# Optimization experiments

Measured on AMD Instinct MI355X. Metric: run time of the kernel, lower is better.

Reference implementation:

```python
import jax, jax.numpy as jnp
import numpy as np

B, C_IN, H, W = 32, 128, 64, 64
C_OUT, KH, KW = 256, 3, 3


def setup_inputs() -> dict:
    key = jax.random.key(0)
    k1, k2, k3 = jax.random.split(key, 3)
    inputs = jax.random.normal(k1, (B, C_IN, H, W), dtype=jnp.float32)
    weights = jax.random.normal(k2, (C_OUT, C_IN, KH, KW), dtype=jnp.float32) * 0.05
    bias = jax.random.normal(k3, (C_OUT, 1), dtype=jnp.float32)
    return {"inputs": inputs, "weights": weights, "bias": bias}


def reference(inputs, weights, bias):
    # Direct 2D valid convolution, stride 1, padding 0 (module default).
    # output[b,o,i,j] = sum_{c,u,v} inputs[b,c,i+u,j+v] * weights[o,c,u,v] + bias[o]
    out = jax.lax.conv_general_dilated(
        inputs, weights,
        window_strides=(1, 1),
        padding="VALID",
        dimension_numbers=("NCHW", "OIHW", "NCHW"),
    )
    # bias has shape (C_out, 1); broadcast per output channel
    return out + bias.reshape(1, -1, 1, 1)
```

## Files before the change

### kernel.cpp

```cpp
#include <hip/hip_runtime.h>
#include <hip/hip_bf16.h>
#include <stdint.h>

#define BB   32
#define CIN  128
#define HH   64
#define WW   64
#define COUT 256
#define OHH  62
#define OWW  62
#define PIX_PER_B (OHH*OWW)
#define NPIX (BB*PIX_PER_B)
#define KTOT (9*CIN)
#define NKT  36
#define SLOT 24576

typedef __bf16 bf16x8 __attribute__((ext_vector_type(8)));
typedef float  f32x4  __attribute__((ext_vector_type(4)));
typedef uint16_t u16x8 __attribute__((ext_vector_type(8)));

__device__ __forceinline__ uint16_t f2bf(float f) {
    uint32_t u = __float_as_uint(f);
    uint32_t r = (u + 0x7FFFu + ((u >> 16) & 1u)) >> 16;
    return (uint16_t)r;
}

__device__ __forceinline__ void gload_lds16(const void* g, void* l) {
    __builtin_amdgcn_global_load_lds(
        (const __attribute__((address_space(1))) uint32_t*)g,
        (__attribute__((address_space(3))) uint32_t*)l, 16, 0, 0);
}

__global__ void __launch_bounds__(256) to_nhwc(const float* __restrict__ in,
                                               uint16_t* __restrict__ out) {
    int slab = blockIdx.x;
    int b = slab >> 6, h = slab & 63;
    int w  = threadIdx.x & 63;
    int cp = threadIdx.x >> 6;
    const float* src = in + (((size_t)b * CIN) * HH + h) * WW + w;
    uint16_t* dst = out + ((size_t)slab * WW + w) * CIN;
    #pragma unroll
    for (int it = 0; it < 4; ++it) {
        int c0 = cp * 32 + it * 8;
        u16x8 v;
        #pragma unroll
        for (int j = 0; j < 8; ++j) v[j] = f2bf(src[(c0 + j) * (HH * WW)]);
        *reinterpret_cast<u16x8*>(dst + c0) = v;
    }
}

__global__ void __launch_bounds__(256) pack_w(const float* __restrict__ w,
                                              uint16_t* __restrict__ out) {
    int idx = blockIdx.x * 256 + threadIdx.x;
    int o = idx / KTOT;
    int k = idx - o * KTOT;
    int uv = k >> 7, c = k & 127;
    out[idx] = f2bf(w[(o * CIN + c) * 9 + uv]);
}

__global__ void __launch_bounds__(256, 2) conv_k32(
        const uint16_t* __restrict__ Xg,
        const uint16_t* __restrict__ Wg,
        const float*    __restrict__ bias,
        float*          __restrict__ out)
{
    __shared__ char lds[3 * SLOT + 1024];
    int* pbase = (int*)(lds + 3 * SLOT);
    int* obase = pbase + 128;

    const int tid  = threadIdx.x;
    const int lane = tid & 63;
    const int wid  = tid >> 6;

    int bid = blockIdx.x;
    int xcd = bid & 7, lid = bid >> 3;
    int nt  = (xcd == 0 ? lid : 121 + (xcd - 1) * 120 + lid);

    if (tid < 128) {
        int n   = nt * 128 + tid;
        int b   = n / PIX_PER_B;
        int rem = n - b * PIX_PER_B;
        int oh  = rem / OWW;
        int ow  = rem - oh * OWW;
        pbase[tid] = ((b * 64 + oh) * 64 + ow) * 128;
        obase[tid] = b * (COUT * PIX_PER_B) + rem;
    }
    __syncthreads();

    const int cs   = (((tid & 3) ^ ((tid >> 3) & 3)) << 4);
    const int ldst = tid * 16;
    const char* aptr0 = (const char*)Wg + ((tid >> 2) + 0)   * (KTOT * 2) + cs;
    const char* aptr1 = (const char*)Wg + ((tid >> 2) + 64)  * (KTOT * 2) + cs;
    const char* aptr2 = (const char*)Wg + ((tid >> 2) + 128) * (KTOT * 2) + cs;
    const char* aptr3 = (const char*)Wg + ((tid >> 2) + 192) * (KTOT * 2) + cs;
    const char* xptr0 = (const char*)Xg + pbase[(tid >> 2)] * 2 + cs;
    const char* xptr1 = (const char*)Xg + pbase[(tid >> 2) + 64] * 2 + cs;

    const int wm = wid >> 1, wn = wid & 1;
    int aro[8], xro[4];
    #pragma unroll
    for (int mi = 0; mi < 8; ++mi) {
        int row = wm * 128 + mi * 16 + (lane & 15);
        aro[mi] = row * 64 + ((((lane >> 4) ^ ((row >> 1) & 3))) << 4);
    }
    #pragma unroll
    for (int nj = 0; nj < 4; ++nj) {
        int row = wn * 64 + nj * 16 + (lane & 15);
        xro[nj] = 16384 + row * 64 + ((((lane >> 4) ^ ((row >> 1) & 3))) << 4);
    }

    f32x4 acc[8][4] = {};

    auto stage = [&](int t, char* dst) {
        int uvv = t >> 2;
        int u   = (uvv * 11) >> 5;
        int v   = uvv - u * 3;
        int xo  = (u << 14) | (v << 8) | ((t & 3) << 6);
        gload_lds16(aptr0 + t * 64, dst + ldst);
        gload_lds16(aptr1 + t * 64, dst + 4096 + ldst);
        gload_lds16(aptr2 + t * 64, dst + 8192 + ldst);
        gload_lds16(aptr3 + t * 64, dst + 12288 + ldst);
        gload_lds16(xptr0 + xo, dst + 16384 + ldst);
        gload_lds16(xptr1 + xo, dst + 20480 + ldst);
    };

#define PHASE(T, S, S2, STG, VMC, BAR) do {                                    \
    char* _slot = lds + (S) * SLOT;                                            \
    if (STG) stage((T) + 2, lds + (S2) * SLOT);                                \
    bf16x8 af[8], xf[4];                                                       \
    _Pragma("unroll") for (int nj = 0; nj < 4; ++nj)                           \
        xf[nj] = *reinterpret_cast<const bf16x8*>(_slot + xro[nj]);            \
    _Pragma("unroll") for (int mi = 0; mi < 8; ++mi)                           \
        af[mi] = *reinterpret_cast<const bf16x8*>(_slot + aro[mi]);            \
    __builtin_amdgcn_s_setprio(1);                                             \
    _Pragma("unroll") for (int mi = 0; mi < 8; ++mi)                           \
      _Pragma("unroll") for (int nj = 0; nj < 4; ++nj)                         \
        acc[mi][nj] = __builtin_amdgcn_mfma_f32_16x16x32_bf16(                 \
            af[mi], xf[nj], acc[mi][nj], 0, 0, 0);                             \
    __builtin_amdgcn_s_setprio(0);                                             \
    if ((VMC) == 1) asm volatile("s_waitcnt vmcnt(6)" ::: "memory");           \
    else if ((VMC) == 2) asm volatile("s_waitcnt vmcnt(0)" ::: "memory");      \
    if (BAR) __builtin_amdgcn_s_barrier();                                     \
} while (0)

    stage(0, lds);
    stage(1, lds + SLOT);
    asm volatile("s_waitcnt vmcnt(6)" ::: "memory");
    __builtin_amdgcn_s_barrier();

    for (int i = 0; i < 11; ++i) {
        PHASE(3 * i + 0, 0, 2, 1, 1, 1);
        PHASE(3 * i + 1, 1, 0, 1, 1, 1);
        PHASE(3 * i + 2, 2, 1, 1, 1, 1);
    }
    PHASE(33, 0, 2, 1, 1, 1);
    PHASE(34, 1, 0, 0, 2, 1);
    PHASE(35, 2, 1, 0, 0, 0);
#undef PHASE

    #pragma unroll
    for (int mi = 0; mi < 8; ++mi) {
        int o = wm * 128 + mi * 16 + ((lane >> 4) << 2);
        #pragma unroll
        for (int reg = 0; reg < 4; ++reg) {
            float bv = bias[o + reg];
            #pragma unroll
            for (int nj = 0; nj < 4; ++nj) {
                int pl = wn * 64 + nj * 16 + (lane & 15);
                out[obase[pl] + (o + reg) * PIX_PER_B] = acc[mi][nj][reg] + bv;
            }
        }
    }
}

__global__ void __launch_bounds__(256) conv_naive(const float* __restrict__ in,
                                                  const float* __restrict__ w,
                                                  const float* __restrict__ bias,
                                                  float* __restrict__ out) {
    long idx = (long)blockIdx.x * 256 + threadIdx.x;
    int t = (int)idx;
    int ow = t % OWW; t /= OWW;
    int oh = t % OHH; t /= OHH;
    int o  = t % COUT;
    int b  = t / COUT;
    float s = bias[o];
    for (int c = 0; c < CIN; ++c)
        for (int u = 0; u < 3; ++u)
            for (int v = 0; v < 3; ++v)
                s += in[((b * CIN + c) * HH + oh + u) * WW + ow + v] *
                     w[((o * CIN + c) * 3 + u) * 3 + v];
    out[idx] = s;
}

extern "C" void kernel_launch(void* const* d_in, const int* in_sizes, int n_in,
                              void* d_out, int out_size, void* d_ws, size_t ws_size,
                              hipStream_t stream) {
    const float* in   = (const float*)d_in[0];
    const float* wt   = (const float*)d_in[1];
    const float* bias = (const float*)d_in[2];
    float* out = (float*)d_out;

    const size_t xg_elems = (size_t)BB * HH * WW * CIN;
    const size_t wg_elems = (size_t)COUT * KTOT;
    const size_t need = (xg_elems + wg_elems) * sizeof(uint16_t);

    if (ws_size < need) {
        long total = (long)BB * COUT * OHH * OWW;
        conv_naive<<<(int)((total + 255) / 256), 256, 0, stream>>>(in, wt, bias, out);
        return;
    }

    uint16_t* Xg = (uint16_t*)d_ws;
    uint16_t* Wg = Xg + xg_elems;

    to_nhwc<<<BB * HH, 256, 0, stream>>>(in, Xg);
    pack_w<<<(COUT * KTOT) / 256, 256, 0, stream>>>(wt, Wg);
    conv_k32<<<NPIX / 128, 256, 0, stream>>>(Xg, Wg, bias, out);
}
```

Baseline: 105.9 us.

## Load weight fragments directly from global into registers, stage only activations in LDS

Weight A-fragments are no longer staged through LDS. Each wave now loads its 8 bf16x8 weight fragments straight from global memory into double-buffered registers, one k-step ahead. LDS slots shrink to hold only the activation tile, and the vmcnt waits are retuned for the new mix of loads. This removes LDS traffic and capacity for weights, at the cost of more VGPRs, plus uncoalesced, redundant global or L2 weight reads, since the two waves sharing wm both fetch the same rows.

After: 183.7 us. 73.5% more time.

```diff
diff --git a/kernel.cpp b/kernel.cpp
--- a/kernel.cpp
+++ b/kernel.cpp
@@ -13,7 +13,7 @@
 #define NPIX (BB*PIX_PER_B)
 #define KTOT (9*CIN)
 #define NKT  36
-#define SLOT 24576
+#define SLOT 8192
 
 typedef __bf16 bf16x8 __attribute__((ext_vector_type(8)));
 typedef float  f32x4  __attribute__((ext_vector_type(4)));
@@ -58,7 +58,7 @@
     out[idx] = f2bf(w[(o * CIN + c) * 9 + uv]);
 }
 
-__global__ void __launch_bounds__(256, 2) conv_k32(
+__global__ void __launch_bounds__(256, 2) conv_areg(
         const uint16_t* __restrict__ Xg,
         const uint16_t* __restrict__ Wg,
         const float*    __restrict__ bias,
@@ -89,74 +89,78 @@
 
     const int cs   = (((tid & 3) ^ ((tid >> 3) & 3)) << 4);
     const int ldst = tid * 16;
-    const char* aptr0 = (const char*)Wg + ((tid >> 2) + 0)   * (KTOT * 2) + cs;
-    const char* aptr1 = (const char*)Wg + ((tid >> 2) + 64)  * (KTOT * 2) + cs;
-    const char* aptr2 = (const char*)Wg + ((tid >> 2) + 128) * (KTOT * 2) + cs;
-    const char* aptr3 = (const char*)Wg + ((tid >> 2) + 192) * (KTOT * 2) + cs;
-    const char* xptr0 = (const char*)Xg + pbase[(tid >> 2)] * 2 + cs;
-    const char* xptr1 = (const char*)Xg + pbase[(tid >> 2) + 64] * 2 + cs;
-
-    const int wm = wid >> 1, wn = wid & 1;
-    int aro[8], xro[4];
-    #pragma unroll
-    for (int mi = 0; mi < 8; ++mi) {
-        int row = wm * 128 + mi * 16 + (lane & 15);
-        aro[mi] = row * 64 + ((((lane >> 4) ^ ((row >> 1) & 3))) << 4);
-    }
-    #pragma unroll
-    for (int nj = 0; nj < 4; ++nj) {
-        int row = wn * 64 + nj * 16 + (lane & 15);
-        xro[nj] = 16384 + row * 64 + ((((lane >> 4) ^ ((row >> 1) & 3))) << 4);
-    }
-
-    f32x4 acc[8][4] = {};
-
-    auto stage = [&](int t, char* dst) {
+    const char* XgB = (const char*)Xg;
+    const char* xptr0 = XgB + pbase[(tid >> 2)] * 2 + cs;
+    const char* xptr1 = XgB + pbase[(tid >> 2) + 64] * 2 + cs;
+
+    auto stageX = [&](int t, char* dst) {
         int uvv = t >> 2;
         int u   = (uvv * 11) >> 5;
         int v   = uvv - u * 3;
         int xo  = (u << 14) | (v << 8) | ((t & 3) << 6);
-        gload_lds16(aptr0 + t * 64, dst + ldst);
-        gload_lds16(aptr1 + t * 64, dst + 4096 + ldst);
-        gload_lds16(aptr2 + t * 64, dst + 8192 + ldst);
-        gload_lds16(aptr3 + t * 64, dst + 12288 + ldst);
-        gload_lds16(xptr0 + xo, dst + 16384 + ldst);
-        gload_lds16(xptr1 + xo, dst + 20480 + ldst);
+        gload_lds16(xptr0 + xo, dst + ldst);
+        gload_lds16(xptr1 + xo, dst + 4096 + ldst);
     };
 
-#define PHASE(T, S, S2, STG, VMC, BAR) do {                                    \
-    char* _slot = lds + (S) * SLOT;                                            \
-    if (STG) stage((T) + 2, lds + (S2) * SLOT);                                \
-    bf16x8 af[8], xf[4];                                                       \
+    const int wm = wid >> 1, wn = wid & 1;
+    const char* ap = (const char*)Wg +
+                     (wm * 128 + (lane & 15)) * (KTOT * 2) + ((lane >> 4) << 4);
+
+    int xro[4];
+    #pragma unroll
+    for (int nj = 0; nj < 4; ++nj) {
+        int row = wn * 64 + nj * 16 + (lane & 15);
+        xro[nj] = row * 64 + ((((lane >> 4) ^ ((row >> 1) & 3))) << 4);
+    }
+
+    f32x4 acc[8][4] = {};
+    bf16x8 afA[8], afB[8];
+
+#define LOADA(T, AF) do {                                                      \
+    const char* _a = ap + (T) * 64;                                            \
+    _Pragma("unroll") for (int mi = 0; mi < 8; ++mi)                           \
+        AF[mi] = *reinterpret_cast<const bf16x8*>(_a + mi * 36864);            \
+} while (0)
+
+#define PH(T, S, S2, AFC, AFN, STG, ALD, VMC, BAR) do {                        \
+    if (STG) stageX((T) + 2, lds + (S2) * SLOT);                               \
+    if (ALD) LOADA((T) + 1, AFN);                                              \
+    bf16x8 xf[4];                                                              \
     _Pragma("unroll") for (int nj = 0; nj < 4; ++nj)                           \
-        xf[nj] = *reinterpret_cast<const bf16x8*>(_slot + xro[nj]);            \
-    _Pragma("unroll") for (int mi = 0; mi < 8; ++mi)                           \
-        af[mi] = *reinterpret_cast<const bf16x8*>(_slot + aro[mi]);            \
+        xf[nj] = *reinterpret_cast<const bf16x8*>(lds + (S) * SLOT + xro[nj]); \
+    asm volatile("s_waitcnt vmcnt(" #VMC ")" ::: "memory");                    \
     __builtin_amdgcn_s_setprio(1);                                             \
     _Pragma("unroll") for (int mi = 0; mi < 8; ++mi)                           \
       _Pragma("unroll") for (int nj = 0; nj < 4; ++nj)                         \
         acc[mi][nj] = __builtin_amdgcn_mfma_f32_16x16x32_bf16(                 \
-            af[mi], xf[nj], acc[mi][nj], 0, 0, 0);                             \
+            AFC[mi], xf[nj], acc[mi][nj], 0, 0, 0);                            \
     __builtin_amdgcn_s_setprio(0);                                             \
-    if ((VMC) == 1) asm volatile("s_waitcnt vmcnt(6)" ::: "memory");           \
-    else if ((VMC) == 2) asm volatile("s_waitcnt vmcnt(0)" ::: "memory");      \
     if (BAR) __builtin_amdgcn_s_barrier();                                     \
 } while (0)
 
-    stage(0, lds);
-    stage(1, lds + SLOT);
-    asm volatile("s_waitcnt vmcnt(6)" ::: "memory");
+    stageX(0, lds);
+    LOADA(0, afA);
+    stageX(1, lds + SLOT);
+    asm volatile("s_waitcnt vmcnt(2)" ::: "memory");
     __builtin_amdgcn_s_barrier();
 
-    for (int i = 0; i < 11; ++i) {
-        PHASE(3 * i + 0, 0, 2, 1, 1, 1);
-        PHASE(3 * i + 1, 1, 0, 1, 1, 1);
-        PHASE(3 * i + 2, 2, 1, 1, 1, 1);
-    }
-    PHASE(33, 0, 2, 1, 1, 1);
-    PHASE(34, 1, 0, 0, 2, 1);
-    PHASE(35, 2, 1, 0, 0, 0);
-#undef PHASE
+    for (int i = 0; i < 5; ++i) {
+        const int t = 6 * i;
+        PH(t + 0, 0, 2, afA, afB, 1, 1, 10, 1);
+        PH(t + 1, 1, 0, afB, afA, 1, 1, 10, 1);
+        PH(t + 2, 2, 1, afA, afB, 1, 1, 10, 1);
+        PH(t + 3, 0, 2, afB, afA, 1, 1, 10, 1);
+        PH(t + 4, 1, 0, afA, afB, 1, 1, 10, 1);
+        PH(t + 5, 2, 1, afB, afA, 1, 1, 10, 1);
+    }
+    PH(30, 0, 2, afA, afB, 1, 1, 10, 1);
+    PH(31, 1, 0, afB, afA, 1, 1, 10, 1);
+    PH(32, 2, 1, afA, afB, 1, 1, 10, 1);
+    PH(33, 0, 2, afB, afA, 1, 1, 10, 1);
+    PH(34, 1, 0, afA, afB, 0, 1,  8, 1);
+    PH(35, 2, 1, afB, afA, 0, 0,  0, 0);
+#undef PH
+#undef LOADA
 
     #pragma unroll
     for (int mi = 0; mi < 8; ++mi) {
@@ -215,5 +219,5 @@
 
     to_nhwc<<<BB * HH, 256, 0, stream>>>(in, Xg);
     pack_w<<<(COUT * KTOT) / 256, 256, 0, stream>>>(wt, Wg);
-    conv_k32<<<NPIX / 128, 256, 0, stream>>>(Xg, Wg, bias, out);
-}
+    conv_areg<<<NPIX / 128, 256, 0, stream>>>(Xg, Wg, bias, out);
+}
```

## Enlarge conv tile to 256x256 pixels with BK=64 and double-buffered LDS

Applied to the files above, without the earlier changes.

The implicit-GEMM conv kernel now uses 512-thread blocks, each covering 256 output channels by 256 pixels, with a 64-wide K step. Pipelining drops from a three-slot to a two-slot LDS ring, with a full vmcnt(0) wait at each step. Each K step now runs two MFMA sub-steps, and the swizzle is widened to 8 chunks. Pixel indices past the end are clamped, and their stores are masked. The aim is to raise operand reuse and halve the number of barriers and K iterations. The cost is about 130KB of LDS per block, so likely only one block fits per CU. Shallower prefetch and block-wide barriers also risk exposing more latency.

Result: slower. 255.0 us (+140.8%).

```diff
diff --git a/kernel.cpp b/kernel.cpp
--- a/kernel.cpp
+++ b/kernel.cpp
@@ -12,8 +12,9 @@
 #define PIX_PER_B (OHH*OWW)
 #define NPIX (BB*PIX_PER_B)
 #define KTOT (9*CIN)
-#define NKT  36
-#define SLOT 24576
+#define NKT2 18
+#define SLOT2 65536
+#define NTBLK 481
 
 typedef __bf16 bf16x8 __attribute__((ext_vector_type(8)));
 typedef float  f32x4  __attribute__((ext_vector_type(4)));
@@ -58,15 +59,15 @@
     out[idx] = f2bf(w[(o * CIN + c) * 9 + uv]);
 }
 
-__global__ void __launch_bounds__(256, 2) conv_k32(
+__global__ void __launch_bounds__(512, 2) conv_bk64(
         const uint16_t* __restrict__ Xg,
         const uint16_t* __restrict__ Wg,
         const float*    __restrict__ bias,
         float*          __restrict__ out)
 {
-    __shared__ char lds[3 * SLOT + 1024];
-    int* pbase = (int*)(lds + 3 * SLOT);
-    int* obase = pbase + 128;
+    __shared__ char lds[2 * SLOT2 + 2048];
+    int* pbase = (int*)(lds + 2 * SLOT2);
+    int* obase = pbase + 256;
 
     const int tid  = threadIdx.x;
     const int lane = tid & 63;
@@ -74,89 +75,113 @@
 
     int bid = blockIdx.x;
     int xcd = bid & 7, lid = bid >> 3;
-    int nt  = (xcd == 0 ? lid : 121 + (xcd - 1) * 120 + lid);
-
-    if (tid < 128) {
-        int n   = nt * 128 + tid;
-        int b   = n / PIX_PER_B;
-        int rem = n - b * PIX_PER_B;
-        int oh  = rem / OWW;
-        int ow  = rem - oh * OWW;
+    int nt  = (xcd == 0) ? lid : 61 + (xcd - 1) * 60 + lid;
+
+    if (tid < 256) {
+        int n     = nt * 256 + tid;
+        int valid = n < NPIX;
+        int nn    = valid ? n : NPIX - 1;
+        int b     = nn / PIX_PER_B;
+        int rem   = nn - b * PIX_PER_B;
+        int oh    = rem / OWW;
+        int ow    = rem - oh * OWW;
         pbase[tid] = ((b * 64 + oh) * 64 + ow) * 128;
-        obase[tid] = b * (COUT * PIX_PER_B) + rem;
+        obase[tid] = valid ? b * (COUT * PIX_PER_B) + rem : -1;
     }
     __syncthreads();
 
-    const int cs   = (((tid & 3) ^ ((tid >> 3) & 3)) << 4);
+    const int cs   = (((tid & 7) ^ ((tid >> 3) & 7)) << 4);
     const int ldst = tid * 16;
-    const char* aptr0 = (const char*)Wg + ((tid >> 2) + 0)   * (KTOT * 2) + cs;
-    const char* aptr1 = (const char*)Wg + ((tid >> 2) + 64)  * (KTOT * 2) + cs;
-    const char* aptr2 = (const char*)Wg + ((tid >> 2) + 128) * (KTOT * 2) + cs;
-    const char* aptr3 = (const char*)Wg + ((tid >> 2) + 192) * (KTOT * 2) + cs;
-    const char* xptr0 = (const char*)Xg + pbase[(tid >> 2)] * 2 + cs;
-    const char* xptr1 = (const char*)Xg + pbase[(tid >> 2) + 64] * 2 + cs;
-
-    const int wm = wid >> 1, wn = wid & 1;
-    int aro[8], xro[4];
+    const char* ap0 = (const char*)Wg + (((tid >> 3) +   0) * (KTOT * 2)) + cs;
+    const char* ap1 = (const char*)Wg + (((tid >> 3) +  64) * (KTOT * 2)) + cs;
+    const char* ap2 = (const char*)Wg + (((tid >> 3) + 128) * (KTOT * 2)) + cs;
+    const char* ap3 = (const char*)Wg + (((tid >> 3) + 192) * (KTOT * 2)) + cs;
+    const char* xp0 = (const char*)Xg + pbase[(tid >> 3) +   0] * 2 + cs;
+    const char* xp1 = (const char*)Xg + pbase[(tid >> 3) +  64] * 2 + cs;
+    const char* xp2 = (const char*)Xg + pbase[(tid >> 3) + 128] * 2 + cs;
+    const char* xp3 = (const char*)Xg + pbase[(tid >> 3) + 192] * 2 + cs;
+
+    auto stage = [&](int t, char* dst) {
+        int uv = t >> 1;
+        int u  = (uv * 11) >> 5;
+        int v  = uv - u * 3;
+        int xo = (u << 14) | (v << 8) | ((t & 1) << 7);
+        gload_lds16(ap0 + t * 128, dst + ldst);
+        gload_lds16(ap1 + t * 128, dst +  8192 + ldst);
+        gload_lds16(ap2 + t * 128, dst + 16384 + ldst);
+        gload_lds16(ap3 + t * 128, dst + 24576 + ldst);
+        gload_lds16(xp0 + xo, dst + 32768 + ldst);
+        gload_lds16(xp1 + xo, dst + 40960 + ldst);
+        gload_lds16(xp2 + xo, dst + 49152 + ldst);
+        gload_lds16(xp3 + xo, dst + 57344 + ldst);
+    };
+
+    const int wm = wid >> 2, wn = wid & 3;
+    int aro[8][2], xro[4][2];
     #pragma unroll
     for (int mi = 0; mi < 8; ++mi) {
         int row = wm * 128 + mi * 16 + (lane & 15);
-        aro[mi] = row * 64 + ((((lane >> 4) ^ ((row >> 1) & 3))) << 4);
+        #pragma unroll
+        for (int ks = 0; ks < 2; ++ks)
+            aro[mi][ks] = row * 128 +
+                (((ks * 4 + (lane >> 4)) ^ (row & 7)) << 4);
     }
     #pragma unroll
     for (int nj = 0; nj < 4; ++nj) {
         int row = wn * 64 + nj * 16 + (lane & 15);
-        xro[nj] = 16384 + row * 64 + ((((lane >> 4) ^ ((row >> 1) & 3))) << 4);
+        #pragma unroll
+        for (int ks = 0; ks < 2; ++ks)
+            xro[nj][ks] = 32768 + row * 128 +
+                (((ks * 4 + (lane >> 4)) ^ (row & 7)) << 4);
     }
 
     f32x4 acc[8][4] = {};
 
-    auto stage = [&](int t, char* dst) {
-        int uvv = t >> 2;
-        int u   = (uvv * 11) >> 5;
-        int v   = uvv - u * 3;
-        int xo  = (u << 14) | (v << 8) | ((t & 3) << 6);
-        gload_lds16(aptr0 + t * 64, dst + ldst);
-        gload_lds16(aptr1 + t * 64, dst + 4096 + ldst);
-        gload_lds16(aptr2 + t * 64, dst + 8192 + ldst);
-        gload_lds16(aptr3 + t * 64, dst + 12288 + ldst);
-        gload_lds16(xptr0 + xo, dst + 16384 + ldst);
-        gload_lds16(xptr1 + xo, dst + 20480 + ldst);
-    };
-
-#define PHASE(T, S, S2, STG, VMC, BAR) do {                                    \
-    char* _slot = lds + (S) * SLOT;                                            \
-    if (STG) stage((T) + 2, lds + (S2) * SLOT);                                \
-    bf16x8 af[8], xf[4];                                                       \
-    _Pragma("unroll") for (int nj = 0; nj < 4; ++nj)                           \
-        xf[nj] = *reinterpret_cast<const bf16x8*>(_slot + xro[nj]);            \
-    _Pragma("unroll") for (int mi = 0; mi < 8; ++mi)                           \
-        af[mi] = *reinterpret_cast<const bf16x8*>(_slot + aro[mi]);            \
-    __builtin_amdgcn_s_setprio(1);                                             \
-    _Pragma("unroll") for (int mi = 0; mi < 8; ++mi)                           \
-      _Pragma("unroll") for (int nj = 0; nj < 4; ++nj)                         \
-        acc[mi][nj] = __builtin_amdgcn_mfma_f32_16x16x32_bf16(                 \
-            af[mi], xf[nj], acc[mi][nj], 0, 0, 0);                             \
-    __builtin_amdgcn_s_setprio(0);                                             \
-    if ((VMC) == 1) asm volatile("s_waitcnt vmcnt(6)" ::: "memory");           \
-    else if ((VMC) == 2) asm volatile("s_waitcnt vmcnt(0)" ::: "memory");      \
+#define PH(T, SB, STG, VMC, BAR) do {                                          \
+    if (STG) stage((T) + 1, lds + (1 - (SB)) * SLOT2);                         \
+    const char* _s = lds + (SB) * SLOT2;                                       \
+    {                                                                          \
+        bf16x8 af[8], xf[4];                                                   \
+        _Pragma("unroll") for (int nj = 0; nj < 4; ++nj)                       \
+            xf[nj] = *reinterpret_cast<const bf16x8*>(_s + xro[nj][0]);        \
+        _Pragma("unroll") for (int mi = 0; mi < 8; ++mi)                       \
+            af[mi] = *reinterpret_cast<const bf16x8*>(_s + aro[mi][0]);        \
+        __builtin_amdgcn_s_setprio(1);                                         \
+        _Pragma("unroll") for (int mi = 0; mi < 8; ++mi)                       \
+          _Pragma("unroll") for (int nj = 0; nj < 4; ++nj)                     \
+            acc[mi][nj] = __builtin_amdgcn_mfma_f32_16x16x32_bf16(             \
+                af[mi], xf[nj], acc[mi][nj], 0, 0, 0);                         \
+        __builtin_amdgcn_s_setprio(0);                                         \
+    }                                                                          \
+    {                                                                          \
+        bf16x8 af[8], xf[4];                                                   \
+        _Pragma("unroll") for (int nj = 0; nj < 4; ++nj)                       \
+            xf[nj] = *reinterpret_cast<const bf16x8*>(_s + xro[nj][1]);        \
+        _Pragma("unroll") for (int mi = 0; mi < 8; ++mi)                       \
+            af[mi] = *reinterpret_cast<const bf16x8*>(_s + aro[mi][1]);        \
+        __builtin_amdgcn_s_setprio(1);                                         \
+        _Pragma("unroll") for (int mi = 0; mi < 8; ++mi)                       \
+          _Pragma("unroll") for (int nj = 0; nj < 4; ++nj)                     \
+            acc[mi][nj] = __builtin_amdgcn_mfma_f32_16x16x32_bf16(             \
+                af[mi], xf[nj], acc[mi][nj], 0, 0, 0);                         \
+        __builtin_amdgcn_s_setprio(0);                                         \
+    }                                                                          \
+    if (VMC) asm volatile("s_waitcnt vmcnt(0)" ::: "memory");                  \
     if (BAR) __builtin_amdgcn_s_barrier();                                     \
 } while (0)
 
     stage(0, lds);
-    stage(1, lds + SLOT);
-    asm volatile("s_waitcnt vmcnt(6)" ::: "memory");
+    stage(1, lds + SLOT2);
+    asm volatile("s_waitcnt vmcnt(8)" ::: "memory");
     __builtin_amdgcn_s_barrier();
 
-    for (int i = 0; i < 11; ++i) {
-        PHASE(3 * i + 0, 0, 2, 1, 1, 1);
-        PHASE(3 * i + 1, 1, 0, 1, 1, 1);
-        PHASE(3 * i + 2, 2, 1, 1, 1, 1);
-    }
-    PHASE(33, 0, 2, 1, 1, 1);
-    PHASE(34, 1, 0, 0, 2, 1);
-    PHASE(35, 2, 1, 0, 0, 0);
-#undef PHASE
+    PH(0, 0, 0, 1, 1);
+    for (int i = 0; i < 8; ++i) {
+        PH(2 * i + 1, 1, 1, 1, 1);
+        PH(2 * i + 2, 0, 1, 1, 1);
+    }
+    PH(17, 1, 0, 0, 0);
+#undef PH
 
     #pragma unroll
     for (int mi = 0; mi < 8; ++mi) {
@@ -167,7 +192,9 @@
             #pragma unroll
             for (int nj = 0; nj < 4; ++nj) {
                 int pl = wn * 64 + nj * 16 + (lane & 15);
-                out[obase[pl] + (o + reg) * PIX_PER_B] = acc[mi][nj][reg] + bv;
+                int ob = obase[pl];
+                if (ob >= 0)
+                    out[ob + (o + reg) * PIX_PER_B] = acc[mi][nj][reg] + bv;
             }
         }
     }
@@ -215,5 +242,5 @@
 
     to_nhwc<<<BB * HH, 256, 0, stream>>>(in, Xg);
     pack_w<<<(COUT * KTOT) / 256, 256, 0, stream>>>(wt, Wg);
-    conv_k32<<<NPIX / 128, 256, 0, stream>>>(Xg, Wg, bias, out);
-}
+    conv_bk64<<<NTBLK, 512, 0, stream>>>(Xg, Wg, bias, out);
+}
```
